# Kernel optimization log

Hardware: AMD Instinct MI355X
Metric: run time of the kernel (lower is better)

Reference implementation:

```python
import jax, jax.numpy as jnp
import numpy as np

VOCAB = 32000
EMB = 256
HID = 512
SEQ = 512
SOS = 1  # word2vec key_to_index['<SOS>']; PAD assumed index 0 and never sampled


def setup_inputs() -> dict:
    key = jax.random.key(0)
    ks = jax.random.split(key, 8)
    k_lstm = 1.0 / np.sqrt(HID)
    k_out = 1.0 / np.sqrt(HID)
    return {
        # token ids in [2, VOCAB) so the PAD-skip branch never triggers
        "input_seq": jax.random.randint(ks[0], (1, SEQ), 2, VOCAB, dtype=jnp.int32),
        "h0": jnp.zeros((1, 1, HID), jnp.float32),
        "c0": jnp.zeros((1, 1, HID), jnp.float32),
        "embedding": jax.random.normal(ks[1], (VOCAB, EMB), jnp.float32) * 0.02,
        "W_ih": jax.random.uniform(ks[2], (4 * HID, EMB), jnp.float32, -k_lstm, k_lstm),
        "W_hh": jax.random.uniform(ks[3], (4 * HID, HID), jnp.float32, -k_lstm, k_lstm),
        "b_ih": jax.random.uniform(ks[4], (4 * HID,), jnp.float32, -k_lstm, k_lstm),
        "b_hh": jax.random.uniform(ks[5], (4 * HID,), jnp.float32, -k_lstm, k_lstm),
        "W_out": jax.random.uniform(ks[6], (VOCAB, HID), jnp.float32, -k_out, k_out),
        "b_out": jax.random.uniform(ks[7], (VOCAB,), jnp.float32, -k_out, k_out),
    }


def reference(input_seq, h0, c0, embedding, W_ih, W_hh, b_ih, b_hh, W_out, b_out):
    # tokens actually fed to the LSTM: <SOS> then the full teacher-forced sequence
    tokens = jnp.concatenate([jnp.array([SOS], jnp.int32), input_seq[0]])  # [S+1]
    emb = embedding[tokens]  # [S+1, E]
    bias = b_ih + b_hh

    def cell(carry, x_t):
        h, c = carry  # [H], [H]
        gates = W_ih @ x_t + W_hh @ h + bias  # [4H], torch gate order i,f,g,o
        i, f, g, o = jnp.split(gates, 4)
        i = jax.nn.sigmoid(i)
        f = jax.nn.sigmoid(f)
        g = jnp.tanh(g)
        o = jax.nn.sigmoid(o)
        c_new = f * c + i * g
        h_new = o * jnp.tanh(c_new)
        return (h_new, c_new), h_new

    (hT, cT), hs = jax.lax.scan(cell, (h0[0, 0], c0[0, 0]), emb)  # hs: [S+1, H]
    logits = hs @ W_out.T + b_out  # [S+1, V] (same math as per-step Linear + cat)
    outputs = logits[None]  # [1, S+1, V]
    return outputs, hT[None, None], cT[None, None]
```

## Files before the change

kernel.cpp:

```cpp
#include <hip/hip_runtime.h>
#include <cmath>

#define VOCAB 32000
#define EMB   256
#define HID   512
#define TLEN  513
#define G4    2048
#define NWG   32
#define SOS   1

typedef unsigned long long u64;
typedef unsigned int uivec4 __attribute__((ext_vector_type(4)));
typedef float f32x4 __attribute__((ext_vector_type(4)));
typedef short bf16x8 __attribute__((ext_vector_type(8)));

__device__ inline float fsig(float x)  { return __builtin_amdgcn_rcpf(1.f + __expf(-x)); }
__device__ inline float ftanh(float x) { return 1.f - 2.f * __builtin_amdgcn_rcpf(__expf(2.f * x) + 1.f); }

__device__ inline void bf16split(float f, short& h, short& l) {
    unsigned u = __float_as_uint(f);
    unsigned r = u + (0x7fffu + ((u >> 16) & 1u));
    unsigned hb = r & 0xffff0000u;
    h = (short)(hb >> 16);
    float res = f - __uint_as_float(hb);
    unsigned u2 = __float_as_uint(res);
    unsigned r2 = u2 + (0x7fffu + ((u2 >> 16) & 1u));
    l = (short)(r2 >> 16);
}

__global__ __launch_bounds__(256) void precompute_gates(
    const int* __restrict__ seq, const float* __restrict__ emb,
    const float* __restrict__ W_ih, const float* __restrict__ b_ih,
    const float* __restrict__ b_hh, float* __restrict__ Xg)
{
    __shared__ __align__(16) float ebuf[16][EMB];
    const int bt = blockIdx.x;
    const int br = blockIdx.y;
    const int tid = threadIdx.x;

    for (int tt = 0; tt < 16; ++tt) {
        int t = bt * 16 + tt;
        if (t < TLEN) {
            int tok = (t == 0) ? SOS : seq[t - 1];
            ebuf[tt][tid] = emb[(size_t)tok * EMB + tid];
        }
    }
    __syncthreads();

    const int row = br * 256 + tid;
    float acc[16];
#pragma unroll
    for (int tt = 0; tt < 16; ++tt) acc[tt] = 0.f;

    const float4* wp = (const float4*)(W_ih + (size_t)row * EMB);
#pragma unroll 4
    for (int k4 = 0; k4 < EMB / 4; ++k4) {
        float4 w = wp[k4];
#pragma unroll
        for (int tt = 0; tt < 16; ++tt) {
            float4 e = *(const float4*)&ebuf[tt][k4 * 4];
            acc[tt] = fmaf(w.x, e.x, fmaf(w.y, e.y, fmaf(w.z, e.z, fmaf(w.w, e.w, acc[tt]))));
        }
    }

    const float bias = b_ih[row] + b_hh[row];
    for (int tt = 0; tt < 16; ++tt) {
        int t = bt * 16 + tt;
        if (t < TLEN) Xg[(size_t)t * G4 + row] = acc[tt] + bias;
    }
}

__global__ __launch_bounds__(256, 1) void lstm_recurrence(
    const float* __restrict__ Xg, const float* __restrict__ W_hh,
    const float* __restrict__ h0, const float* __restrict__ c0,
    float* __restrict__ hs, u64* pk, u64* pf,
    float* __restrict__ out_hT, float* __restrict__ out_cT)
{
    __shared__ __align__(16) float hbuf[HID];
    __shared__ float pbuf[2][256];

    const int bx = blockIdx.x;
    if (bx & 7) return;
    const int wg  = bx >> 3;
    const int tid = threadIdx.x;
    const int wv  = tid >> 6;
    const int ln  = tid & 63;
    const int q   = ln >> 4;
    const int j   = ln & 15;
    const int row = q * HID + wg * 16 + j;

    float4 wreg[32];
    const float4* wp = (const float4*)(W_hh + (size_t)row * HID + wv * 128);
#pragma unroll
    for (int i = 0; i < 32; ++i) wreg[i] = wp[i];

    float c = (tid < 16) ? c0[wg * 16 + tid] : 0.f;
    {
        float2 h2 = *(const float2*)&h0[tid * 2];
        hbuf[tid * 2]     = h2.x;
        hbuf[tid * 2 + 1] = h2.y;
    }
    __syncthreads();

    bool usefast = true;

    for (int t = 0; t < TLEN; ++t) {
        float xg0 = 0.f, xg1 = 0.f, xg2 = 0.f, xg3 = 0.f;
        if (tid < 16) {
            const float* xp = Xg + (size_t)t * G4 + wg * 16 + tid;
            xg0 = xp[0]; xg1 = xp[512]; xg2 = xp[1024]; xg3 = xp[1536];
        }

        if (t > 0) {
            const unsigned tt = (unsigned)t;
            const size_t off = (size_t)(t & 1) * HID + 2 * tid;
            uivec4 r;
            bool got = false;
            if (usefast) {
                u64 fa = (u64)(uintptr_t)(pf + off);
                const int K = (t == 1) ? 128 : 64;
                for (int it = 0; it < K; ++it) {
                    asm volatile("global_load_dwordx4 %0, %1, off sc0\n\t"
                                 "s_waitcnt vmcnt(0)" : "=v"(r) : "v"(fa));
                    if (r.y == tt && r.w == tt) { got = true; break; }
                }
                if (__ballot(got ? 1 : 0) != ~0ull) usefast = false;
            }
            if (!got) {
                u64 sa = (u64)(uintptr_t)(pk + off);
                do {
                    asm volatile("global_load_dwordx4 %0, %1, off sc0 sc1\n\t"
                                 "s_waitcnt vmcnt(0)" : "=v"(r) : "v"(sa));
                } while (r.y != tt || r.w != tt);
            }
            hbuf[2 * tid]     = __uint_as_float(r.x);
            hbuf[2 * tid + 1] = __uint_as_float(r.z);
            asm volatile("s_waitcnt lgkmcnt(0)" ::: "memory");
        }

        float acc8[8];
#pragma unroll
        for (int i = 0; i < 8; ++i) acc8[i] = 0.f;
#pragma unroll
        for (int i = 0; i < 32; ++i) {
            float4 w4 = wreg[i];
            float4 h4 = *(const float4*)&hbuf[wv * 128 + i * 4];
            acc8[i & 7] = fmaf(w4.x, h4.x, fmaf(w4.y, h4.y,
                          fmaf(w4.z, h4.z, fmaf(w4.w, h4.w, acc8[i & 7]))));
        }
        pbuf[t & 1][tid] = ((acc8[0] + acc8[1]) + (acc8[2] + acc8[3]))
                         + ((acc8[4] + acc8[5]) + (acc8[6] + acc8[7]));
        __syncthreads();

        if (tid < 16) {
            const float* pb = pbuf[t & 1];
            float gi = pb[tid]      + pb[64 + tid]  + pb[128 + tid] + pb[192 + tid] + xg0;
            float gf = pb[16 + tid] + pb[80 + tid]  + pb[144 + tid] + pb[208 + tid] + xg1;
            float gg = pb[32 + tid] + pb[96 + tid]  + pb[160 + tid] + pb[224 + tid] + xg2;
            float go = pb[48 + tid] + pb[112 + tid] + pb[176 + tid] + pb[240 + tid] + xg3;
            float i_ = fsig(gi);
            float f_ = fsig(gf);
            float g_ = ftanh(gg);
            float o_ = fsig(go);
            c = fmaf(f_, c, i_ * g_);
            float h_ = o_ * ftanh(c);
            if (t < TLEN - 1) {
                u64 word = ((u64)(unsigned)(t + 1) << 32) | (u64)__float_as_uint(h_);
                size_t po = (size_t)((t + 1) & 1) * HID + wg * 16 + tid;
                u64 faddr = (u64)(uintptr_t)(pf + po);
                asm volatile("global_store_dwordx2 %0, %1, off sc0"
                             :: "v"(faddr), "v"(word) : "memory");
                __hip_atomic_store(&pk[po], word, __ATOMIC_RELAXED, __HIP_MEMORY_SCOPE_AGENT);
            } else {
                out_hT[wg * 16 + tid] = h_;
                out_cT[wg * 16 + tid] = c;
            }
            hs[(size_t)t * HID + wg * 16 + tid] = h_;
        }
    }
}

#define GLDT 40

__global__ __launch_bounds__(256, 2) void out_gemm_mfma(
    const float* __restrict__ hs, const float* __restrict__ W_out,
    const float* __restrict__ b_out, float* __restrict__ out)
{
    __shared__ __align__(16) short Ah[128][GLDT];
    __shared__ __align__(16) short Al[128][GLDT];
    __shared__ __align__(16) short Bh[128][GLDT];
    __shared__ __align__(16) short Bl[128][GLDT];

    const int tb = blockIdx.x;
    const int vb = blockIdx.y;
    const int tid = threadIdx.x;
    const int w   = tid >> 6;
    const int l   = tid & 63;
    const int l15 = l & 15;
    const int lg  = l >> 4;
    const int m0 = tb * 128, n0 = vb * 128;

    const int sr = tid >> 1;
    const int kh = (tid & 1) * 16;

    f32x4 acc[2][8];
#pragma unroll
    for (int s = 0; s < 2; ++s)
#pragma unroll
        for (int cc = 0; cc < 8; ++cc) acc[s][cc] = (f32x4){0.f, 0.f, 0.f, 0.f};

    for (int k0 = 0; k0 < HID; k0 += 32) {
        {
            int trow = m0 + sr;
            float4 fa0 = make_float4(0.f,0.f,0.f,0.f), fa1 = fa0, fa2 = fa0, fa3 = fa0;
            if (trow < TLEN) {
                const float4* ap = (const float4*)(hs + (size_t)trow * HID + k0 + kh);
                fa0 = ap[0]; fa1 = ap[1]; fa2 = ap[2]; fa3 = ap[3];
            }
            float fv[16] = { fa0.x,fa0.y,fa0.z,fa0.w, fa1.x,fa1.y,fa1.z,fa1.w,
                             fa2.x,fa2.y,fa2.z,fa2.w, fa3.x,fa3.y,fa3.z,fa3.w };
#pragma unroll
            for (int g = 0; g < 2; ++g) {
                union { short s[8]; bf16x8 v; } ph, pl;
#pragma unroll
                for (int e = 0; e < 8; ++e) bf16split(fv[g * 8 + e], ph.s[e], pl.s[e]);
                *(bf16x8*)&Ah[sr][kh + 8 * g] = ph.v;
                *(bf16x8*)&Al[sr][kh + 8 * g] = pl.v;
            }
        }
        {
            const float4* bp = (const float4*)(W_out + (size_t)(n0 + sr) * HID + k0 + kh);
            float4 fb0 = bp[0], fb1 = bp[1], fb2 = bp[2], fb3 = bp[3];
            float fv[16] = { fb0.x,fb0.y,fb0.z,fb0.w, fb1.x,fb1.y,fb1.z,fb1.w,
                             fb2.x,fb2.y,fb2.z,fb2.w, fb3.x,fb3.y,fb3.z,fb3.w };
#pragma unroll
            for (int g = 0; g < 2; ++g) {
                union { short s[8]; bf16x8 v; } ph, pl;
#pragma unroll
                for (int e = 0; e < 8; ++e) bf16split(fv[g * 8 + e], ph.s[e], pl.s[e]);
                *(bf16x8*)&Bh[sr][kh + 8 * g] = ph.v;
                *(bf16x8*)&Bl[sr][kh + 8 * g] = pl.v;
            }
        }
        __syncthreads();

        bf16x8 ah[2], al2[2];
#pragma unroll
        for (int s = 0; s < 2; ++s) {
            ah[s]  = *(const bf16x8*)&Ah[32 * w + 16 * s + l15][8 * lg];
            al2[s] = *(const bf16x8*)&Al[32 * w + 16 * s + l15][8 * lg];
        }
#pragma unroll
        for (int cc = 0; cc < 8; ++cc) {
            bf16x8 bh = *(const bf16x8*)&Bh[16 * cc + l15][8 * lg];
            bf16x8 bl = *(const bf16x8*)&Bl[16 * cc + l15][8 * lg];
#pragma unroll
            for (int s = 0; s < 2; ++s) {
                acc[s][cc] = __builtin_amdgcn_mfma_f32_16x16x32_bf16(ah[s],  bh, acc[s][cc], 0, 0, 0);
                acc[s][cc] = __builtin_amdgcn_mfma_f32_16x16x32_bf16(ah[s],  bl, acc[s][cc], 0, 0, 0);
                acc[s][cc] = __builtin_amdgcn_mfma_f32_16x16x32_bf16(al2[s], bh, acc[s][cc], 0, 0, 0);
            }
        }
        __syncthreads();
    }

#pragma unroll
    for (int cc = 0; cc < 8; ++cc) {
        int col = n0 + 16 * cc + l15;
        float bo = b_out[col];
#pragma unroll
        for (int s = 0; s < 2; ++s) {
            int rbase = m0 + 32 * w + 16 * s + lg * 4;
#pragma unroll
            for (int r = 0; r < 4; ++r) {
                int trow = rbase + r;
                if (trow < TLEN) out[(size_t)trow * VOCAB + col] = acc[s][cc][r] + bo;
            }
        }
    }
}

extern "C" void kernel_launch(void* const* d_in, const int* in_sizes, int n_in,
                              void* d_out, int out_size, void* d_ws, size_t ws_size,
                              hipStream_t stream)
{
    const int*   seq   = (const int*)  d_in[0];
    const float* h0    = (const float*)d_in[1];
    const float* c0    = (const float*)d_in[2];
    const float* emb   = (const float*)d_in[3];
    const float* W_ih  = (const float*)d_in[4];
    const float* W_hh  = (const float*)d_in[5];
    const float* b_ih  = (const float*)d_in[6];
    const float* b_hh  = (const float*)d_in[7];
    const float* W_out = (const float*)d_in[8];
    const float* b_out = (const float*)d_in[9];

    float* out_logits = (float*)d_out;
    float* out_hT     = out_logits + (size_t)TLEN * VOCAB;
    float* out_cT     = out_hT + HID;

    float* Xg = (float*)d_ws;
    float* hs = Xg + (size_t)TLEN * G4;
    u64*   pk = (u64*)(hs + (size_t)TLEN * HID);
    u64*   pf = pk + 2 * HID;

    hipMemsetAsync(pk, 0, 4 * HID * sizeof(u64), stream);
    precompute_gates<<<dim3(33, 8), 256, 0, stream>>>(seq, emb, W_ih, b_ih, b_hh, Xg);
    lstm_recurrence<<<249, 256, 0, stream>>>(Xg, W_hh, h0, c0, hs, pk, pf, out_hT, out_cT);
    out_gemm_mfma<<<dim3(5, 250), 256, 0, stream>>>(hs, W_out, b_out, out_logits);
}
```

Measured before the change: 924.8 us.

## Launch recurrence with exactly NWG blocks and pin W_hh slices in registers

The recurrence kernel now launches exactly 32 workgroups instead of 249 blocks, most of which exited at once. The earlier launch appeared to spread the active blocks across different XCDs or CUs by taking only every eighth block index. The W_hh slice is now held in 32 named vector registers, fenced with empty asm so the compiler keeps them resident, and the dot product is written out by hand. The first-step fast-poll budget is raised to 512. The risk is a different placement of workgroups across XCDs, which could change the latency of cross-workgroup flag polling.

```diff
diff --git a/kernel.cpp b/kernel.cpp
--- a/kernel.cpp
+++ b/kernel.cpp
@@ -16,6 +16,9 @@
 
 __device__ inline float fsig(float x)  { return __builtin_amdgcn_rcpf(1.f + __expf(-x)); }
 __device__ inline float ftanh(float x) { return 1.f - 2.f * __builtin_amdgcn_rcpf(__expf(2.f * x) + 1.f); }
+__device__ inline float fma4(f32x4 w, f32x4 h, float a) {
+    return fmaf(w[0], h[0], fmaf(w[1], h[1], fmaf(w[2], h[2], fmaf(w[3], h[3], a))));
+}
 
 __device__ inline void bf16split(float f, short& h, short& l) {
     unsigned u = __float_as_uint(f);
@@ -79,9 +82,7 @@
     __shared__ __align__(16) float hbuf[HID];
     __shared__ float pbuf[2][256];
 
-    const int bx = blockIdx.x;
-    if (bx & 7) return;
-    const int wg  = bx >> 3;
+    const int wg  = blockIdx.x;
     const int tid = threadIdx.x;
     const int wv  = tid >> 6;
     const int ln  = tid & 63;
@@ -89,10 +90,23 @@
     const int j   = ln & 15;
     const int row = q * HID + wg * 16 + j;
 
-    float4 wreg[32];
-    const float4* wp = (const float4*)(W_hh + (size_t)row * HID + wv * 128);
-#pragma unroll
-    for (int i = 0; i < 32; ++i) wreg[i] = wp[i];
+    const f32x4* wp4 = (const f32x4*)(W_hh + (size_t)row * HID + wv * 128);
+    f32x4 w00=wp4[0],  w01=wp4[1],  w02=wp4[2],  w03=wp4[3];
+    f32x4 w04=wp4[4],  w05=wp4[5],  w06=wp4[6],  w07=wp4[7];
+    f32x4 w08=wp4[8],  w09=wp4[9],  w10=wp4[10], w11=wp4[11];
+    f32x4 w12=wp4[12], w13=wp4[13], w14=wp4[14], w15=wp4[15];
+    f32x4 w16=wp4[16], w17=wp4[17], w18=wp4[18], w19=wp4[19];
+    f32x4 w20=wp4[20], w21=wp4[21], w22=wp4[22], w23=wp4[23];
+    f32x4 w24=wp4[24], w25=wp4[25], w26=wp4[26], w27=wp4[27];
+    f32x4 w28=wp4[28], w29=wp4[29], w30=wp4[30], w31=wp4[31];
+    asm volatile("" : "+v"(w00), "+v"(w01), "+v"(w02), "+v"(w03));
+    asm volatile("" : "+v"(w04), "+v"(w05), "+v"(w06), "+v"(w07));
+    asm volatile("" : "+v"(w08), "+v"(w09), "+v"(w10), "+v"(w11));
+    asm volatile("" : "+v"(w12), "+v"(w13), "+v"(w14), "+v"(w15));
+    asm volatile("" : "+v"(w16), "+v"(w17), "+v"(w18), "+v"(w19));
+    asm volatile("" : "+v"(w20), "+v"(w21), "+v"(w22), "+v"(w23));
+    asm volatile("" : "+v"(w24), "+v"(w25), "+v"(w26), "+v"(w27));
+    asm volatile("" : "+v"(w28), "+v"(w29), "+v"(w30), "+v"(w31));
 
     float c = (tid < 16) ? c0[wg * 16 + tid] : 0.f;
     {
@@ -118,7 +132,7 @@
             bool got = false;
             if (usefast) {
                 u64 fa = (u64)(uintptr_t)(pf + off);
-                const int K = (t == 1) ? 128 : 64;
+                const int K = (t == 1) ? 512 : 64;
                 for (int it = 0; it < K; ++it) {
                     asm volatile("global_load_dwordx4 %0, %1, off sc0\n\t"
                                  "s_waitcnt vmcnt(0)" : "=v"(r) : "v"(fa));
@@ -138,18 +152,26 @@
             asm volatile("s_waitcnt lgkmcnt(0)" ::: "memory");
         }
 
-        float acc8[8];
-#pragma unroll
-        for (int i = 0; i < 8; ++i) acc8[i] = 0.f;
-#pragma unroll
-        for (int i = 0; i < 32; ++i) {
-            float4 w4 = wreg[i];
-            float4 h4 = *(const float4*)&hbuf[wv * 128 + i * 4];
-            acc8[i & 7] = fmaf(w4.x, h4.x, fmaf(w4.y, h4.y,
-                          fmaf(w4.z, h4.z, fmaf(w4.w, h4.w, acc8[i & 7]))));
-        }
-        pbuf[t & 1][tid] = ((acc8[0] + acc8[1]) + (acc8[2] + acc8[3]))
-                         + ((acc8[4] + acc8[5]) + (acc8[6] + acc8[7]));
+        const f32x4* hp = (const f32x4*)&hbuf[wv * 128];
+        float a0 = 0.f, a1 = 0.f, a2 = 0.f, a3 = 0.f;
+        float a4 = 0.f, a5 = 0.f, a6 = 0.f, a7 = 0.f;
+        a0 = fma4(w00, hp[0],  a0); a1 = fma4(w01, hp[1],  a1);
+        a2 = fma4(w02, hp[2],  a2); a3 = fma4(w03, hp[3],  a3);
+        a4 = fma4(w04, hp[4],  a4); a5 = fma4(w05, hp[5],  a5);
+        a6 = fma4(w06, hp[6],  a6); a7 = fma4(w07, hp[7],  a7);
+        a0 = fma4(w08, hp[8],  a0); a1 = fma4(w09, hp[9],  a1);
+        a2 = fma4(w10, hp[10], a2); a3 = fma4(w11, hp[11], a3);
+        a4 = fma4(w12, hp[12], a4); a5 = fma4(w13, hp[13], a5);
+        a6 = fma4(w14, hp[14], a6); a7 = fma4(w15, hp[15], a7);
+        a0 = fma4(w16, hp[16], a0); a1 = fma4(w17, hp[17], a1);
+        a2 = fma4(w18, hp[18], a2); a3 = fma4(w19, hp[19], a3);
+        a4 = fma4(w20, hp[20], a4); a5 = fma4(w21, hp[21], a5);
+        a6 = fma4(w22, hp[22], a6); a7 = fma4(w23, hp[23], a7);
+        a0 = fma4(w24, hp[24], a0); a1 = fma4(w25, hp[25], a1);
+        a2 = fma4(w26, hp[26], a2); a3 = fma4(w27, hp[27], a3);
+        a4 = fma4(w28, hp[28], a4); a5 = fma4(w29, hp[29], a5);
+        a6 = fma4(w30, hp[30], a6); a7 = fma4(w31, hp[31], a7);
+        pbuf[t & 1][tid] = ((a0 + a1) + (a2 + a3)) + ((a4 + a5) + (a6 + a7));
         __syncthreads();
 
         if (tid < 16) {
@@ -306,6 +328,6 @@
 
     hipMemsetAsync(pk, 0, 4 * HID * sizeof(u64), stream);
     precompute_gates<<<dim3(33, 8), 256, 0, stream>>>(seq, emb, W_ih, b_ih, b_hh, Xg);
-    lstm_recurrence<<<249, 256, 0, stream>>>(Xg, W_hh, h0, c0, hs, pk, pf, out_hT, out_cT);
+    lstm_recurrence<<<NWG, 256, 0, stream>>>(Xg, W_hh, h0, c0, hs, pk, pf, out_hT, out_cT);
     out_gemm_mfma<<<dim3(5, 250), 256, 0, stream>>>(hs, W_out, b_out, out_logits);
 }
```

New measurement: 1.009 ms. +9.1%, slower.

## Simplify LSTM cross-workgroup sync to a single coherent flag buffer with atomic exchange

Applied to the files above, without the earlier changes.

Removes the dual-buffer fast/slow polling scheme, in which writers stored h to a non-coherent fast buffer plus a coherent buffer and readers polled the fast one first. Now there is one coherent buffer, written with an atomic exchange and polled with sc0 sc1 loads. The launch drops from 249 blocks, of which only every eighth did work (likely chosen to spread them across XCDs), to 32 contiguous blocks. The dot-product accumulation is also restructured, which may shift register scheduling. The risk is that the workgroups may now share XCD L2 differently, and polling only the coherent buffer could add latency on every timestep.

```diff
diff --git a/kernel.cpp b/kernel.cpp
--- a/kernel.cpp
+++ b/kernel.cpp
@@ -16,6 +16,9 @@
 
 __device__ inline float fsig(float x)  { return __builtin_amdgcn_rcpf(1.f + __expf(-x)); }
 __device__ inline float ftanh(float x) { return 1.f - 2.f * __builtin_amdgcn_rcpf(__expf(2.f * x) + 1.f); }
+__device__ inline float fma4(f32x4 w, f32x4 h, float a) {
+    return fmaf(w[0], h[0], fmaf(w[1], h[1], fmaf(w[2], h[2], fmaf(w[3], h[3], a))));
+}
 
 __device__ inline void bf16split(float f, short& h, short& l) {
     unsigned u = __float_as_uint(f);
@@ -73,15 +76,13 @@
 __global__ __launch_bounds__(256, 1) void lstm_recurrence(
     const float* __restrict__ Xg, const float* __restrict__ W_hh,
     const float* __restrict__ h0, const float* __restrict__ c0,
-    float* __restrict__ hs, u64* pk, u64* pf,
+    float* __restrict__ hs, u64* pk,
     float* __restrict__ out_hT, float* __restrict__ out_cT)
 {
     __shared__ __align__(16) float hbuf[HID];
     __shared__ float pbuf[2][256];
 
-    const int bx = blockIdx.x;
-    if (bx & 7) return;
-    const int wg  = bx >> 3;
+    const int wg  = blockIdx.x;
     const int tid = threadIdx.x;
     const int wv  = tid >> 6;
     const int ln  = tid & 63;
@@ -89,8 +90,8 @@
     const int j   = ln & 15;
     const int row = q * HID + wg * 16 + j;
 
-    float4 wreg[32];
-    const float4* wp = (const float4*)(W_hh + (size_t)row * HID + wv * 128);
+    f32x4 wreg[32];
+    const f32x4* wp = (const f32x4*)(W_hh + (size_t)row * HID + wv * 128);
 #pragma unroll
     for (int i = 0; i < 32; ++i) wreg[i] = wp[i];
 
@@ -102,8 +103,6 @@
     }
     __syncthreads();
 
-    bool usefast = true;
-
     for (int t = 0; t < TLEN; ++t) {
         float xg0 = 0.f, xg1 = 0.f, xg2 = 0.f, xg3 = 0.f;
         if (tid < 16) {
@@ -113,43 +112,32 @@
 
         if (t > 0) {
             const unsigned tt = (unsigned)t;
-            const size_t off = (size_t)(t & 1) * HID + 2 * tid;
+            u64 sa = (u64)(uintptr_t)(pk + (size_t)(t & 1) * HID + 2 * tid);
             uivec4 r;
-            bool got = false;
-            if (usefast) {
-                u64 fa = (u64)(uintptr_t)(pf + off);
-                const int K = (t == 1) ? 128 : 64;
-                for (int it = 0; it < K; ++it) {
-                    asm volatile("global_load_dwordx4 %0, %1, off sc0\n\t"
-                                 "s_waitcnt vmcnt(0)" : "=v"(r) : "v"(fa));
-                    if (r.y == tt && r.w == tt) { got = true; break; }
-                }
-                if (__ballot(got ? 1 : 0) != ~0ull) usefast = false;
-            }
-            if (!got) {
-                u64 sa = (u64)(uintptr_t)(pk + off);
-                do {
-                    asm volatile("global_load_dwordx4 %0, %1, off sc0 sc1\n\t"
-                                 "s_waitcnt vmcnt(0)" : "=v"(r) : "v"(sa));
-                } while (r.y != tt || r.w != tt);
-            }
+            do {
+                asm volatile("global_load_dwordx4 %0, %1, off sc0 sc1\n\t"
+                             "s_waitcnt vmcnt(0)" : "=v"(r) : "v"(sa));
+            } while (r.y != tt || r.w != tt);
             hbuf[2 * tid]     = __uint_as_float(r.x);
             hbuf[2 * tid + 1] = __uint_as_float(r.z);
             asm volatile("s_waitcnt lgkmcnt(0)" ::: "memory");
         }
 
-        float acc8[8];
-#pragma unroll
-        for (int i = 0; i < 8; ++i) acc8[i] = 0.f;
-#pragma unroll
-        for (int i = 0; i < 32; ++i) {
-            float4 w4 = wreg[i];
-            float4 h4 = *(const float4*)&hbuf[wv * 128 + i * 4];
-            acc8[i & 7] = fmaf(w4.x, h4.x, fmaf(w4.y, h4.y,
-                          fmaf(w4.z, h4.z, fmaf(w4.w, h4.w, acc8[i & 7]))));
-        }
-        pbuf[t & 1][tid] = ((acc8[0] + acc8[1]) + (acc8[2] + acc8[3]))
-                         + ((acc8[4] + acc8[5]) + (acc8[6] + acc8[7]));
+        float a0 = 0.f, a1 = 0.f, a2 = 0.f, a3 = 0.f;
+        float a4 = 0.f, a5 = 0.f, a6 = 0.f, a7 = 0.f;
+        const f32x4* hp = (const f32x4*)&hbuf[wv * 128];
+#pragma unroll
+        for (int i = 0; i < 32; i += 8) {
+            a0 = fma4(wreg[i],     hp[i],     a0);
+            a1 = fma4(wreg[i + 1], hp[i + 1], a1);
+            a2 = fma4(wreg[i + 2], hp[i + 2], a2);
+            a3 = fma4(wreg[i + 3], hp[i + 3], a3);
+            a4 = fma4(wreg[i + 4], hp[i + 4], a4);
+            a5 = fma4(wreg[i + 5], hp[i + 5], a5);
+            a6 = fma4(wreg[i + 6], hp[i + 6], a6);
+            a7 = fma4(wreg[i + 7], hp[i + 7], a7);
+        }
+        pbuf[t & 1][tid] = ((a0 + a1) + (a2 + a3)) + ((a4 + a5) + (a6 + a7));
         __syncthreads();
 
         if (tid < 16) {
@@ -166,11 +154,9 @@
             float h_ = o_ * ftanh(c);
             if (t < TLEN - 1) {
                 u64 word = ((u64)(unsigned)(t + 1) << 32) | (u64)__float_as_uint(h_);
-                size_t po = (size_t)((t + 1) & 1) * HID + wg * 16 + tid;
-                u64 faddr = (u64)(uintptr_t)(pf + po);
-                asm volatile("global_store_dwordx2 %0, %1, off sc0"
-                             :: "v"(faddr), "v"(word) : "memory");
-                __hip_atomic_store(&pk[po], word, __ATOMIC_RELAXED, __HIP_MEMORY_SCOPE_AGENT);
+                (void)__hip_atomic_exchange(
+                    &pk[(size_t)((t + 1) & 1) * HID + wg * 16 + tid], word,
+                    __ATOMIC_RELAXED, __HIP_MEMORY_SCOPE_AGENT);
             } else {
                 out_hT[wg * 16 + tid] = h_;
                 out_cT[wg * 16 + tid] = c;
@@ -302,10 +288,9 @@
     float* Xg = (float*)d_ws;
     float* hs = Xg + (size_t)TLEN * G4;
     u64*   pk = (u64*)(hs + (size_t)TLEN * HID);
-    u64*   pf = pk + 2 * HID;
-
-    hipMemsetAsync(pk, 0, 4 * HID * sizeof(u64), stream);
+
+    (void)hipMemsetAsync(pk, 0, 2 * HID * sizeof(u64), stream);
     precompute_gates<<<dim3(33, 8), 256, 0, stream>>>(seq, emb, W_ih, b_ih, b_hh, Xg);
-    lstm_recurrence<<<249, 256, 0, stream>>>(Xg, W_hh, h0, c0, hs, pk, pf, out_hT, out_cT);
+    lstm_recurrence<<<NWG, 256, 0, stream>>>(Xg, W_hh, h0, c0, hs, pk, out_hT, out_cT);
     out_gemm_mfma<<<dim3(5, 250), 256, 0, stream>>>(hs, W_out, b_out, out_logits);
 }
```

Result: slower. 957.4 us (+3.5%).
